# Performance work log

Hardware: AMD Instinct MI355X
Metric: run time of the kernel (lower is better)

The kernel has to match this reference:

```python
import jax, jax.numpy as jnp
import numpy as np

B, T, C, H = 8, 2048, 1024, 128

def setup_inputs() -> dict:
    key = jax.random.key(0)
    k1, k2, k3, k4 = jax.random.split(key, 4)
    scale = 0.02
    return {
        "x": jax.random.normal(k1, (B, T, C), dtype=jnp.float32),
        "Wq": jax.random.normal(k2, (C, H), dtype=jnp.float32) * scale,
        "Wk": jax.random.normal(k3, (C, H), dtype=jnp.float32) * scale,
        "Wv": jax.random.normal(k4, (C, H), dtype=jnp.float32) * scale,
    }

def reference(x, Wq, Wk, Wv):
    # Single causal attention head (dropout p=0.0 -> identity)
    q = jnp.einsum('btc,ch->bth', x, Wq)
    k = jnp.einsum('btc,ch->bth', x, Wk)
    v = jnp.einsum('btc,ch->bth', x, Wv)
    head_size = k.shape[-1]
    scores = jnp.einsum('bth,bsh->bts', q, k) / jnp.sqrt(jnp.asarray(head_size, q.dtype))  # [B,T,T]
    causal = jnp.tril(jnp.ones((scores.shape[1], scores.shape[2]), dtype=bool))
    scores = jnp.where(causal, scores, -jnp.inf)
    weights = jax.nn.softmax(scores, axis=-1)
    context = jnp.einsum('bts,bsh->bth', weights, v)  # [B,T,H]
    return context
```

## Files before the change

kernel.cpp:

```cpp
#include <hip/hip_runtime.h>

typedef __bf16 bf16x8 __attribute__((ext_vector_type(8)));
typedef float f32x4 __attribute__((ext_vector_type(4)));
typedef float fv4 __attribute__((ext_vector_type(4)));

#define B_ 8
#define T_ 2048
#define C_ 1024
#define H_ 128

__global__ __launch_bounds__(256) void prep_kernel(
    const float* __restrict__ Wq, const float* __restrict__ Wk,
    const float* __restrict__ Wv, __bf16* __restrict__ Wt)
{
  __shared__ __bf16 ldsT[128 * 136];
  const int tid = threadIdx.x;
  const int k0 = blockIdx.x * 128;
  const int wsel = blockIdx.y;
  const float* W = wsel == 0 ? Wq : (wsel == 1 ? Wk : Wv);
#pragma unroll
  for (int i = 0; i < 16; ++i) {
    int fidx = tid + 256 * i;
    int k = fidx >> 5, h4 = (fidx & 31) << 2;
    fv4 w = *(const fv4*)(W + (size_t)(k0 + k) * H_ + h4);
#pragma unroll
    for (int j = 0; j < 4; ++j) ldsT[(h4 + j) * 136 + k] = (__bf16)w[j];
  }
  __syncthreads();
#pragma unroll
  for (int i = 0; i < 8; ++i) {
    int sidx = tid + 256 * i;
    int h = sidx >> 4, c8 = (sidx & 15) << 3;
    *(bf16x8*)(Wt + (size_t)wsel * H_ * C_ + (size_t)h * C_ + k0 + c8) =
        *(const bf16x8*)&ldsT[h * 136 + c8];
  }
}

__global__ __launch_bounds__(256) void proj_kernel(
    const float* __restrict__ x, const __bf16* __restrict__ Wt,
    __bf16* __restrict__ Qw, __bf16* __restrict__ Kw, __bf16* __restrict__ Vtw)
{
  __shared__ __align__(16) __bf16 ldsA[32 * 40];
  __shared__ __align__(16) __bf16 ldsB[384 * 40];
  const int tid = threadIdx.x;
  const int wave = tid >> 6, lane = tid & 63;
  const int q4 = lane >> 4, l16 = lane & 15;
  const int bt0 = blockIdx.x * 32;

  const f32x4 zero4 = {0.f, 0.f, 0.f, 0.f};
  f32x4 acc[2][6];
#pragma unroll
  for (int mt = 0; mt < 2; ++mt)
#pragma unroll
    for (int nt = 0; nt < 6; ++nt) acc[mt][nt] = zero4;

  fv4 xa0, xa1;
  bf16x8 wpre[6];
  const int arow = tid >> 2, acol8 = (tid & 3) << 3;
  if (tid < 128) {
    const float* s = x + (size_t)(bt0 + arow) * C_ + acol8;
    xa0 = *(const fv4*)s;
    xa1 = *(const fv4*)(s + 4);
  }
#pragma unroll
  for (int i = 0; i < 6; ++i) {
    int idx = tid + 256 * i;
    int col = idx >> 2, k8 = (idx & 3) << 3;
    wpre[i] = *(const bf16x8*)(Wt + (size_t)col * C_ + k8);
  }

  for (int kc = 0; kc < C_; kc += 32) {
    if (tid < 128) {
      bf16x8 v;
#pragma unroll
      for (int j = 0; j < 4; ++j) { v[j] = (__bf16)xa0[j]; v[4 + j] = (__bf16)xa1[j]; }
      *(bf16x8*)&ldsA[arow * 40 + acol8] = v;
    }
#pragma unroll
    for (int i = 0; i < 6; ++i) {
      int idx = tid + 256 * i;
      int col = idx >> 2, k8 = (idx & 3) << 3;
      *(bf16x8*)&ldsB[col * 40 + k8] = wpre[i];
    }
    __syncthreads();
    const int kn = (kc + 32 < C_) ? kc + 32 : kc;
    if (tid < 128) {
      const float* s = x + (size_t)(bt0 + arow) * C_ + kn + acol8;
      xa0 = *(const fv4*)s;
      xa1 = *(const fv4*)(s + 4);
    }
#pragma unroll
    for (int i = 0; i < 6; ++i) {
      int idx = tid + 256 * i;
      int col = idx >> 2, k8 = (idx & 3) << 3;
      wpre[i] = *(const bf16x8*)(Wt + (size_t)col * C_ + kn + k8);
    }
    bf16x8 af[2];
#pragma unroll
    for (int mt = 0; mt < 2; ++mt)
      af[mt] = *(const bf16x8*)&ldsA[(mt * 16 + l16) * 40 + q4 * 8];
#pragma unroll
    for (int nt = 0; nt < 6; ++nt) {
      bf16x8 bf = *(const bf16x8*)&ldsB[(wave * 96 + nt * 16 + l16) * 40 + q4 * 8];
#pragma unroll
      for (int mt = 0; mt < 2; ++mt)
        acc[mt][nt] = __builtin_amdgcn_mfma_f32_16x16x32_bf16(af[mt], bf, acc[mt][nt], 0, 0, 0);
    }
    __syncthreads();
  }

  const int b = bt0 >> 11, t0 = bt0 & (T_ - 1);
#pragma unroll
  for (int mt = 0; mt < 2; ++mt)
#pragma unroll
    for (int nt = 0; nt < 6; ++nt) {
      int gcol = wave * 96 + nt * 16 + l16;
#pragma unroll
      for (int r = 0; r < 4; ++r) {
        int row = bt0 + mt * 16 + q4 * 4 + r;
        float v = acc[mt][nt][r];
        if (gcol < 128) Qw[(size_t)row * H_ + gcol] = (__bf16)v;
        else if (gcol < 256) Kw[(size_t)row * H_ + (gcol - 128)] = (__bf16)v;
        else {
          int tl = mt * 16 + q4 * 4 + r;
          ldsB[(gcol - 256) * 40 + tl] = (__bf16)v;
        }
      }
    }
  __syncthreads();
#pragma unroll
  for (int i = 0; i < 2; ++i) {
    int idx = tid + 256 * i;
    int h = idx >> 2, t8 = (idx & 3) << 3;
    *(bf16x8*)(Vtw + ((size_t)b * H_ + h) * T_ + t0 + t8) =
        *(const bf16x8*)&ldsB[h * 40 + t8];
  }
}

__global__ __launch_bounds__(256) void attn_split(
    const __bf16* __restrict__ Q, const __bf16* __restrict__ K,
    const __bf16* __restrict__ Vt, float* __restrict__ PO,
    float* __restrict__ Pl, float* __restrict__ out)
{
  __shared__ __align__(16) __bf16 ldsK[64 * 136];
  __shared__ __align__(16) __bf16 ldsV[128 * 72];
  __shared__ __align__(16) __bf16 ldsP[4][16 * 72];
  const int tid = threadIdx.x;
  const int wave = tid >> 6, lane = tid & 63;
  const int q4 = lane >> 4, l16 = lane & 15;
  const int b = blockIdx.y;
  int rem = blockIdx.x, qb = 0;
  while (rem >= (qb >> 3) + 1) { rem -= (qb >> 3) + 1; ++qb; }
  const int c = rem;
  const int tstart = c << 3;
  const int tend = min(tstart + 8, qb + 1);
  const int nch = (qb >> 3) + 1;
  const int qw = qb * 64 + wave * 16;
  const __bf16* Qb = Q + (size_t)b * T_ * H_;
  const __bf16* Kb = K + (size_t)b * T_ * H_;
  const __bf16* Vb = Vt + (size_t)b * H_ * T_;
  __bf16* ldsPw = &ldsP[wave][0];

  bf16x8 qf[4];
#pragma unroll
  for (int kc = 0; kc < 4; ++kc)
    qf[kc] = *(const bf16x8*)(Qb + (size_t)(qw + l16) * H_ + kc * 32 + q4 * 8);

  const f32x4 zero4 = {0.f, 0.f, 0.f, 0.f};
  f32x4 o[8];
#pragma unroll
  for (int nt = 0; nt < 8; ++nt) o[nt] = zero4;
  float lsum[4] = {0.f, 0.f, 0.f, 0.f};

  bf16x8 kp[4], vp[4];
#pragma unroll
  for (int i = 0; i < 4; ++i) {
    int idx = tid + 256 * i;
    int krow = idx >> 4, kcol8 = (idx & 15) << 3;
    kp[i] = *(const bf16x8*)(Kb + (size_t)(tstart * 64 + krow) * H_ + kcol8);
    int vrow = idx >> 3, vcol8 = (idx & 7) << 3;
    vp[i] = *(const bf16x8*)(Vb + (size_t)vrow * T_ + tstart * 64 + vcol8);
  }

  for (int t = tstart; t < tend; ++t) {
    const int kv0 = t << 6;
#pragma unroll
    for (int i = 0; i < 4; ++i) {
      int idx = tid + 256 * i;
      int krow = idx >> 4, kcol8 = (idx & 15) << 3;
      *(bf16x8*)&ldsK[krow * 136 + kcol8] = kp[i];
      int vrow = idx >> 3, vcol8 = (idx & 7) << 3;
      *(bf16x8*)&ldsV[vrow * 72 + vcol8] = vp[i];
    }
    __syncthreads();
    const int kvn = (t + 1 < tend) ? (kv0 + 64) : kv0;
#pragma unroll
    for (int i = 0; i < 4; ++i) {
      int idx = tid + 256 * i;
      int krow = idx >> 4, kcol8 = (idx & 15) << 3;
      kp[i] = *(const bf16x8*)(Kb + (size_t)(kvn + krow) * H_ + kcol8);
      int vrow = idx >> 3, vcol8 = (idx & 7) << 3;
      vp[i] = *(const bf16x8*)(Vb + (size_t)vrow * T_ + kvn + vcol8);
    }

    f32x4 s[4];
#pragma unroll
    for (int nt = 0; nt < 4; ++nt) s[nt] = zero4;
#pragma unroll
    for (int nt = 0; nt < 4; ++nt)
#pragma unroll
      for (int kc = 0; kc < 4; ++kc) {
        bf16x8 kf = *(const bf16x8*)&ldsK[(nt * 16 + l16) * 136 + kc * 32 + q4 * 8];
        s[nt] = __builtin_amdgcn_mfma_f32_16x16x32_bf16(qf[kc], kf, s[nt], 0, 0, 0);
      }

    if (t == qb) {
#pragma unroll
      for (int r = 0; r < 4; ++r) {
        const int grow = qw + q4 * 4 + r;
#pragma unroll
        for (int nt = 0; nt < 4; ++nt) {
          int col = kv0 + nt * 16 + l16;
          float p = (col <= grow) ? __expf(s[nt][r] * 0.08838834764831845f) : 0.f;
          lsum[r] += p;
          ldsPw[(q4 * 4 + r) * 72 + nt * 16 + l16] = (__bf16)p;
        }
      }
    } else {
#pragma unroll
      for (int r = 0; r < 4; ++r)
#pragma unroll
        for (int nt = 0; nt < 4; ++nt) {
          float p = __expf(s[nt][r] * 0.08838834764831845f);
          lsum[r] += p;
          ldsPw[(q4 * 4 + r) * 72 + nt * 16 + l16] = (__bf16)p;
        }
    }
#pragma unroll
    for (int kc2 = 0; kc2 < 2; ++kc2) {
      bf16x8 pf = *(const bf16x8*)&ldsPw[l16 * 72 + kc2 * 32 + q4 * 8];
#pragma unroll
      for (int nt = 0; nt < 8; ++nt) {
        bf16x8 vf = *(const bf16x8*)&ldsV[(nt * 16 + l16) * 72 + kc2 * 32 + q4 * 8];
        o[nt] = __builtin_amdgcn_mfma_f32_16x16x32_bf16(pf, vf, o[nt], 0, 0, 0);
      }
    }
    __syncthreads();
  }

  float lred[4];
#pragma unroll
  for (int r = 0; r < 4; ++r) {
    float l = lsum[r];
    l += __shfl_xor(l, 1);
    l += __shfl_xor(l, 2);
    l += __shfl_xor(l, 4);
    l += __shfl_xor(l, 8);
    lred[r] = l;
  }

  if (nch == 1) {
#pragma unroll
    for (int r = 0; r < 4; ++r) lred[r] = 1.f / lred[r];
#pragma unroll
    for (int nt = 0; nt < 8; ++nt)
#pragma unroll
      for (int r = 0; r < 4; ++r) {
        int row = qw + q4 * 4 + r;
        out[((size_t)b * T_ + row) * H_ + nt * 16 + l16] = o[nt][r] * lred[r];
      }
  } else {
    const int slot = b * 80 + qb + max(qb - 8, 0) + max(qb - 16, 0) + max(qb - 24, 0) + c;
    float* POs = PO + (size_t)slot * 8192;
#pragma unroll
    for (int nt = 0; nt < 8; ++nt)
#pragma unroll
      for (int r = 0; r < 4; ++r)
        POs[(wave * 16 + q4 * 4 + r) * 128 + nt * 16 + l16] = o[nt][r];
    if (l16 == 0)
#pragma unroll
      for (int r = 0; r < 4; ++r)
        Pl[slot * 64 + wave * 16 + q4 * 4 + r] = lred[r];
  }
}

__global__ __launch_bounds__(256) void attn_combine(
    const float* __restrict__ PO, const float* __restrict__ Pl,
    float* __restrict__ out)
{
  const int qb = blockIdx.x + 8;
  const int b = blockIdx.y;
  const int nch = (qb >> 3) + 1;
  const int slot0 = b * 80 + qb + max(qb - 8, 0) + max(qb - 16, 0) + max(qb - 24, 0);
  const int tid = threadIdx.x;
  const int row = tid >> 2, h0 = (tid & 3) << 5;
  const fv4 z4 = {0.f, 0.f, 0.f, 0.f};
  fv4 oacc[8];
#pragma unroll
  for (int j = 0; j < 8; ++j) oacc[j] = z4;
  float lacc = 0.f;
  for (int cc = 0; cc < nch; ++cc) {
    const int slot = slot0 + cc;
    lacc += Pl[slot * 64 + row];
    const float* Ps = PO + (size_t)slot * 8192 + row * 128 + h0;
#pragma unroll
    for (int j = 0; j < 8; ++j) oacc[j] += *(const fv4*)(Ps + 4 * j);
  }
  const float inv = 1.f / lacc;
  float* op = out + ((size_t)b * T_ + qb * 64 + row) * H_ + h0;
#pragma unroll
  for (int j = 0; j < 8; ++j) {
    fv4 v = oacc[j] * inv;
    *(fv4*)(op + 4 * j) = v;
  }
}

__global__ __launch_bounds__(256) void attn_mono(
    const __bf16* __restrict__ Q, const __bf16* __restrict__ K,
    const __bf16* __restrict__ Vt, float* __restrict__ out)
{
  __shared__ __align__(16) __bf16 ldsK[64 * 136];
  __shared__ __align__(16) __bf16 ldsV[128 * 72];
  __shared__ __align__(16) __bf16 ldsP[4][16 * 72];
  const int tid = threadIdx.x;
  const int wave = tid >> 6, lane = tid & 63;
  const int q4 = lane >> 4, l16 = lane & 15;
  const int qb = blockIdx.x, b = blockIdx.y;
  const int qw = qb * 64 + wave * 16;
  const __bf16* Qb = Q + (size_t)b * T_ * H_;
  const __bf16* Kb = K + (size_t)b * T_ * H_;
  const __bf16* Vb = Vt + (size_t)b * H_ * T_;
  __bf16* ldsPw = &ldsP[wave][0];

  bf16x8 qf[4];
#pragma unroll
  for (int kc = 0; kc < 4; ++kc)
    qf[kc] = *(const bf16x8*)(Qb + (size_t)(qw + l16) * H_ + kc * 32 + q4 * 8);

  const f32x4 zero4 = {0.f, 0.f, 0.f, 0.f};
  f32x4 o[8];
#pragma unroll
  for (int nt = 0; nt < 8; ++nt) o[nt] = zero4;
  float lsum[4] = {0.f, 0.f, 0.f, 0.f};
  const int ntile = qb + 1;

  bf16x8 kp[4], vp[4];
#pragma unroll
  for (int i = 0; i < 4; ++i) {
    int idx = tid + 256 * i;
    int krow = idx >> 4, kcol8 = (idx & 15) << 3;
    kp[i] = *(const bf16x8*)(Kb + (size_t)krow * H_ + kcol8);
    int vrow = idx >> 3, vcol8 = (idx & 7) << 3;
    vp[i] = *(const bf16x8*)(Vb + (size_t)vrow * T_ + vcol8);
  }

  for (int t = 0; t < ntile; ++t) {
    const int kv0 = t << 6;
#pragma unroll
    for (int i = 0; i < 4; ++i) {
      int idx = tid + 256 * i;
      int krow = idx >> 4, kcol8 = (idx & 15) << 3;
      *(bf16x8*)&ldsK[krow * 136 + kcol8] = kp[i];
      int vrow = idx >> 3, vcol8 = (idx & 7) << 3;
      *(bf16x8*)&ldsV[vrow * 72 + vcol8] = vp[i];
    }
    __syncthreads();
    int kvn = (t + 1 < ntile) ? (kv0 + 64) : kv0;
#pragma unroll
    for (int i = 0; i < 4; ++i) {
      int idx = tid + 256 * i;
      int krow = idx >> 4, kcol8 = (idx & 15) << 3;
      kp[i] = *(const bf16x8*)(Kb + (size_t)(kvn + krow) * H_ + kcol8);
      int vrow = idx >> 3, vcol8 = (idx & 7) << 3;
      vp[i] = *(const bf16x8*)(Vb + (size_t)vrow * T_ + kvn + vcol8);
    }
    f32x4 s[4];
#pragma unroll
    for (int nt = 0; nt < 4; ++nt) s[nt] = zero4;
#pragma unroll
    for (int nt = 0; nt < 4; ++nt)
#pragma unroll
      for (int kc = 0; kc < 4; ++kc) {
        bf16x8 kf = *(const bf16x8*)&ldsK[(nt * 16 + l16) * 136 + kc * 32 + q4 * 8];
        s[nt] = __builtin_amdgcn_mfma_f32_16x16x32_bf16(qf[kc], kf, s[nt], 0, 0, 0);
      }
#pragma unroll
    for (int r = 0; r < 4; ++r) {
      const int grow = qw + q4 * 4 + r;
#pragma unroll
      for (int nt = 0; nt < 4; ++nt) {
        int col = kv0 + nt * 16 + l16;
        float p = (col <= grow) ? __expf(s[nt][r] * 0.08838834764831845f) : 0.f;
        lsum[r] += p;
        ldsPw[(q4 * 4 + r) * 72 + nt * 16 + l16] = (__bf16)p;
      }
    }
#pragma unroll
    for (int kc2 = 0; kc2 < 2; ++kc2) {
      bf16x8 pf = *(const bf16x8*)&ldsPw[l16 * 72 + kc2 * 32 + q4 * 8];
#pragma unroll
      for (int nt = 0; nt < 8; ++nt) {
        bf16x8 vf = *(const bf16x8*)&ldsV[(nt * 16 + l16) * 72 + kc2 * 32 + q4 * 8];
        o[nt] = __builtin_amdgcn_mfma_f32_16x16x32_bf16(pf, vf, o[nt], 0, 0, 0);
      }
    }
    __syncthreads();
  }
  float rinv[4];
#pragma unroll
  for (int r = 0; r < 4; ++r) {
    float l = lsum[r];
    l += __shfl_xor(l, 1);
    l += __shfl_xor(l, 2);
    l += __shfl_xor(l, 4);
    l += __shfl_xor(l, 8);
    rinv[r] = 1.f / l;
  }
#pragma unroll
  for (int nt = 0; nt < 8; ++nt)
#pragma unroll
    for (int r = 0; r < 4; ++r) {
      int row = qw + q4 * 4 + r;
      out[((size_t)b * T_ + row) * H_ + nt * 16 + l16] = o[nt][r] * rinv[r];
    }
}

extern "C" void kernel_launch(void* const* d_in, const int* in_sizes, int n_in,
                              void* d_out, int out_size, void* d_ws, size_t ws_size,
                              hipStream_t stream) {
  const float* x  = (const float*)d_in[0];
  const float* Wq = (const float*)d_in[1];
  const float* Wk = (const float*)d_in[2];
  const float* Wv = (const float*)d_in[3];
  __bf16* ws = (__bf16*)d_ws;
  __bf16* Qw  = ws;
  __bf16* Kw  = ws + (size_t)B_ * T_ * H_;
  __bf16* Vtw = ws + (size_t)2 * B_ * T_ * H_;
  __bf16* Wt  = ws + (size_t)3 * B_ * T_ * H_;
  const size_t bf16_bytes = 13369344;
  float* PO = (float*)((char*)d_ws + bf16_bytes);
  float* Pl = PO + (size_t)640 * 64 * 128;
  const size_t need = bf16_bytes + ((size_t)640 * 64 * 128 + 640 * 64) * 4;
  float* out = (float*)d_out;

  prep_kernel<<<dim3(8, 3), 256, 0, stream>>>(Wq, Wk, Wv, Wt);
  proj_kernel<<<512, 256, 0, stream>>>(x, Wt, Qw, Kw, Vtw);
  if (ws_size >= need) {
    attn_split<<<dim3(80, 8), 256, 0, stream>>>(Qw, Kw, Vtw, PO, Pl, out);
    attn_combine<<<dim3(24, 8), 256, 0, stream>>>(PO, Pl, out);
  } else {
    attn_mono<<<dim3(32, 8), 256, 0, stream>>>(Qw, Kw, Vtw, out);
  }
}
```

Measured before the change: 174.2 us.

## Double-buffer projection prefetch, store split partials in bf16, widen combine grid

The projection kernel now prefetches two K-chunks ahead into register slots, aiming to hide global-load latency behind the MFMA work. The attention split kernel writes its unnormalized partial outputs as bf16 instead of fp32, which halves the partial-buffer traffic. The combine kernel is split four ways per query block, giving more blocks and one 16-byte load per slot per thread. The costs are higher register pressure in the projection and some precision loss in the partial sums.

```diff
diff --git a/kernel.cpp b/kernel.cpp
--- a/kernel.cpp
+++ b/kernel.cpp
@@ -54,46 +54,52 @@
 #pragma unroll
     for (int nt = 0; nt < 6; ++nt) acc[mt][nt] = zero4;
 
-  fv4 xa0, xa1;
-  bf16x8 wpre[6];
   const int arow = tid >> 2, acol8 = (tid & 3) << 3;
-  if (tid < 128) {
-    const float* s = x + (size_t)(bt0 + arow) * C_ + acol8;
-    xa0 = *(const fv4*)s;
-    xa1 = *(const fv4*)(s + 4);
-  }
-#pragma unroll
-  for (int i = 0; i < 6; ++i) {
-    int idx = tid + 256 * i;
-    int col = idx >> 2, k8 = (idx & 3) << 3;
-    wpre[i] = *(const bf16x8*)(Wt + (size_t)col * C_ + k8);
-  }
-
-  for (int kc = 0; kc < C_; kc += 32) {
+
+  fv4 xa[2][2];
+  bf16x8 wp[2][6];
+#pragma unroll
+  for (int slot = 0; slot < 2; ++slot) {
+    const int kb = slot * 32;
+    if (tid < 128) {
+      const float* s = x + (size_t)(bt0 + arow) * C_ + kb + acol8;
+      xa[slot][0] = *(const fv4*)s;
+      xa[slot][1] = *(const fv4*)(s + 4);
+    }
+#pragma unroll
+    for (int i = 0; i < 6; ++i) {
+      int idx = tid + 256 * i;
+      int col = idx >> 2, k8 = (idx & 3) << 3;
+      wp[slot][i] = *(const bf16x8*)(Wt + (size_t)col * C_ + kb + k8);
+    }
+  }
+
+  for (int c = 0; c < 32; ++c) {
+    const int s = c & 1;
     if (tid < 128) {
       bf16x8 v;
 #pragma unroll
-      for (int j = 0; j < 4; ++j) { v[j] = (__bf16)xa0[j]; v[4 + j] = (__bf16)xa1[j]; }
+      for (int j = 0; j < 4; ++j) { v[j] = (__bf16)xa[s][0][j]; v[4 + j] = (__bf16)xa[s][1][j]; }
       *(bf16x8*)&ldsA[arow * 40 + acol8] = v;
     }
 #pragma unroll
     for (int i = 0; i < 6; ++i) {
       int idx = tid + 256 * i;
       int col = idx >> 2, k8 = (idx & 3) << 3;
-      *(bf16x8*)&ldsB[col * 40 + k8] = wpre[i];
-    }
-    __syncthreads();
-    const int kn = (kc + 32 < C_) ? kc + 32 : kc;
+      *(bf16x8*)&ldsB[col * 40 + k8] = wp[s][i];
+    }
+    __syncthreads();
+    const int kn = (c + 2 < 32) ? (c + 2) * 32 : c * 32;
     if (tid < 128) {
-      const float* s = x + (size_t)(bt0 + arow) * C_ + kn + acol8;
-      xa0 = *(const fv4*)s;
-      xa1 = *(const fv4*)(s + 4);
+      const float* sp = x + (size_t)(bt0 + arow) * C_ + kn + acol8;
+      xa[s][0] = *(const fv4*)sp;
+      xa[s][1] = *(const fv4*)(sp + 4);
     }
 #pragma unroll
     for (int i = 0; i < 6; ++i) {
       int idx = tid + 256 * i;
       int col = idx >> 2, k8 = (idx & 3) << 3;
-      wpre[i] = *(const bf16x8*)(Wt + (size_t)col * C_ + kn + k8);
+      wp[s][i] = *(const bf16x8*)(Wt + (size_t)col * C_ + kn + k8);
     }
     bf16x8 af[2];
 #pragma unroll
@@ -139,7 +145,7 @@
 
 __global__ __launch_bounds__(256) void attn_split(
     const __bf16* __restrict__ Q, const __bf16* __restrict__ K,
-    const __bf16* __restrict__ Vt, float* __restrict__ PO,
+    const __bf16* __restrict__ Vt, __bf16* __restrict__ PO,
     float* __restrict__ Pl, float* __restrict__ out)
 {
   __shared__ __align__(16) __bf16 ldsK[64 * 136];
@@ -271,12 +277,12 @@
       }
   } else {
     const int slot = b * 80 + qb + max(qb - 8, 0) + max(qb - 16, 0) + max(qb - 24, 0) + c;
-    float* POs = PO + (size_t)slot * 8192;
+    __bf16* POs = PO + (size_t)slot * 8192;
 #pragma unroll
     for (int nt = 0; nt < 8; ++nt)
 #pragma unroll
       for (int r = 0; r < 4; ++r)
-        POs[(wave * 16 + q4 * 4 + r) * 128 + nt * 16 + l16] = o[nt][r];
+        POs[(wave * 16 + q4 * 4 + r) * 128 + nt * 16 + l16] = (__bf16)o[nt][r];
     if (l16 == 0)
 #pragma unroll
       for (int r = 0; r < 4; ++r)
@@ -285,34 +291,33 @@
 }
 
 __global__ __launch_bounds__(256) void attn_combine(
-    const float* __restrict__ PO, const float* __restrict__ Pl,
+    const __bf16* __restrict__ PO, const float* __restrict__ Pl,
     float* __restrict__ out)
 {
-  const int qb = blockIdx.x + 8;
+  const int qb = 8 + (blockIdx.x >> 2);
+  const int seg = blockIdx.x & 3;
   const int b = blockIdx.y;
   const int nch = (qb >> 3) + 1;
   const int slot0 = b * 80 + qb + max(qb - 8, 0) + max(qb - 16, 0) + max(qb - 24, 0);
   const int tid = threadIdx.x;
-  const int row = tid >> 2, h0 = (tid & 3) << 5;
-  const fv4 z4 = {0.f, 0.f, 0.f, 0.f};
-  fv4 oacc[8];
-#pragma unroll
-  for (int j = 0; j < 8; ++j) oacc[j] = z4;
+  const int rloc = seg * 16 + (tid >> 4);
+  const int col8 = (tid & 15) << 3;
+  float oacc[8] = {0.f};
   float lacc = 0.f;
   for (int cc = 0; cc < nch; ++cc) {
     const int slot = slot0 + cc;
-    lacc += Pl[slot * 64 + row];
-    const float* Ps = PO + (size_t)slot * 8192 + row * 128 + h0;
-#pragma unroll
-    for (int j = 0; j < 8; ++j) oacc[j] += *(const fv4*)(Ps + 4 * j);
+    lacc += Pl[slot * 64 + rloc];
+    bf16x8 v = *(const bf16x8*)(PO + (size_t)slot * 8192 + rloc * 128 + col8);
+#pragma unroll
+    for (int j = 0; j < 8; ++j) oacc[j] += (float)v[j];
   }
   const float inv = 1.f / lacc;
-  float* op = out + ((size_t)b * T_ + qb * 64 + row) * H_ + h0;
-#pragma unroll
-  for (int j = 0; j < 8; ++j) {
-    fv4 v = oacc[j] * inv;
-    *(fv4*)(op + 4 * j) = v;
-  }
+  float* op = out + ((size_t)b * T_ + qb * 64 + rloc) * H_ + col8;
+  fv4 v0, v1;
+#pragma unroll
+  for (int j = 0; j < 4; ++j) { v0[j] = oacc[j] * inv; v1[j] = oacc[4 + j] * inv; }
+  *(fv4*)op = v0;
+  *(fv4*)(op + 4) = v1;
 }
 
 __global__ __launch_bounds__(256) void attn_mono(
@@ -437,17 +442,17 @@
   __bf16* Kw  = ws + (size_t)B_ * T_ * H_;
   __bf16* Vtw = ws + (size_t)2 * B_ * T_ * H_;
   __bf16* Wt  = ws + (size_t)3 * B_ * T_ * H_;
-  const size_t bf16_bytes = 13369344;
-  float* PO = (float*)((char*)d_ws + bf16_bytes);
-  float* Pl = PO + (size_t)640 * 64 * 128;
-  const size_t need = bf16_bytes + ((size_t)640 * 64 * 128 + 640 * 64) * 4;
+  const size_t bf16_elems = 6684672;
+  __bf16* PO = ws + bf16_elems;
+  float* Pl = (float*)(ws + bf16_elems + (size_t)640 * 8192);
+  const size_t need = bf16_elems * 2 + (size_t)640 * 8192 * 2 + (size_t)640 * 64 * 4;
   float* out = (float*)d_out;
 
   prep_kernel<<<dim3(8, 3), 256, 0, stream>>>(Wq, Wk, Wv, Wt);
   proj_kernel<<<512, 256, 0, stream>>>(x, Wt, Qw, Kw, Vtw);
   if (ws_size >= need) {
     attn_split<<<dim3(80, 8), 256, 0, stream>>>(Qw, Kw, Vtw, PO, Pl, out);
-    attn_combine<<<dim3(24, 8), 256, 0, stream>>>(PO, Pl, out);
+    attn_combine<<<dim3(96, 8), 256, 0, stream>>>(PO, Pl, out);
   } else {
     attn_mono<<<dim3(32, 8), 256, 0, stream>>>(Qw, Kw, Vtw, out);
   }
```

Measured after the change: 170.8 us. No clear change (-2.0%).
